# Kernel tuning notes

Measured on AMD Instinct MI355X. Metric: run time of the kernel, lower is better.

Reference implementation:

```python
import jax, jax.numpy as jnp
import numpy as np

N = 8192
IN_C, HID_C, OUT_C = 128, 256, 128


def setup_inputs() -> dict:
    key = jax.random.key(0)
    ks = jax.random.split(key, 6)
    return {
        "x": jax.random.normal(ks[0], (N, IN_C), dtype=jnp.float32),
        "adaptive_params": jax.random.normal(ks[1], (N, N), dtype=jnp.float32),
        "W1": jax.random.normal(ks[2], (IN_C, HID_C), dtype=jnp.float32) * (1.0 / np.sqrt(IN_C)),
        "b1": jax.random.normal(ks[3], (HID_C,), dtype=jnp.float32) * 0.01,
        "W2": jax.random.normal(ks[4], (HID_C, OUT_C), dtype=jnp.float32) * (1.0 / np.sqrt(HID_C)),
        "b2": jax.random.normal(ks[5], (OUT_C,), dtype=jnp.float32) * 0.01,
    }


def _normalized_adj(adaptive_params):
    # initial_adj = I; A = sigmoid(sym(I + P)) where sym(M) = (M + M^T)/2
    n = adaptive_params.shape[0]
    eye = jnp.eye(n, dtype=adaptive_params.dtype)
    sym = eye + 0.5 * (adaptive_params + adaptive_params.T)
    A = jax.nn.sigmoid(sym)
    # sigmoid > 0 everywhere -> edge_index covers all N^2 pairs (dense graph).
    # PyG gcn_norm (add_self_loops=True, fill_value=1.0): A_hat = A + I,
    # then symmetric degree normalization D^-1/2 A_hat D^-1/2.
    A_hat = A + eye
    dinv = jax.lax.rsqrt(jnp.sum(A_hat, axis=1))  # [N]
    return A_hat * dinv[:, None] * dinv[None, :]


def reference(x, adaptive_params, W1, b1, W2, b2):
    A_norm = _normalized_adj(adaptive_params)          # [N, N]
    h = jax.nn.relu(A_norm @ (x @ W1) + b1)            # [N, HID_C]
    out = A_norm @ (h @ W2) + b2                       # [N, OUT_C]
    return out
```

## Files before the change

### kernel.cpp

```cpp
#include <hip/hip_runtime.h>
#include <hip/hip_bf16.h>
#include <cstdint>

typedef unsigned short u16;
typedef unsigned short u16x4 __attribute__((ext_vector_type(4)));
typedef unsigned short u16x8 __attribute__((ext_vector_type(8)));
typedef _Float16 f16x8 __attribute__((ext_vector_type(8)));
typedef float f32x4 __attribute__((ext_vector_type(4)));

constexpr int NN   = 8192;
constexpr int INC  = 128;
constexpr int HIDC = 256;
constexpr int OUTC = 128;
constexpr int KSPLIT = 8;

__device__ __forceinline__ u16 f2h(float f) {
    _Float16 h = (_Float16)f;
    return __builtin_bit_cast(u16, h);
}
__device__ __forceinline__ float h2f(u16 u) {
    return (float)__builtin_bit_cast(_Float16, u);
}
__device__ __forceinline__ float fast_sigmoid(float z) {
    float e;
    asm("v_exp_f32 %0, %1" : "=v"(e) : "v"(z * -1.44269504088896f));
    float s;
    asm("v_rcp_f32 %0, %1" : "=v"(s) : "v"(1.0f + e));
    return s;
}

typedef __attribute__((address_space(1))) const void* gptr_t;
typedef __attribute__((address_space(3))) void* sptr_t;
#define GLD16(g, s) __builtin_amdgcn_global_load_lds((gptr_t)(g), (sptr_t)(s), 16, 0, 0)

__global__ __launch_bounds__(512, 4) void k_adj(const float* __restrict__ P,
                                                u16* __restrict__ AH,
                                                float* __restrict__ psum,
                                                const float* __restrict__ W2,
                                                u16* __restrict__ W2T) {
    const int t = threadIdx.x;
    if (blockIdx.x == 0) {
        for (int e = t; e < OUTC * HIDC; e += 512) {
            int c = e >> 8, k = e & 255;
            W2T[c * HIDC + k] = f2h(W2[k * OUTC + c]);
        }
        return;
    }
    int bid = blockIdx.x - 1;
    int bi, bj;
    if (bid >= 2016)      { bi = bj = bid - 2016; }
    else if (bid >= 1984) { bi = 31; bj = 32 + (bid - 1984); }
    else {
        int u = bid >> 6, v = bid & 63;
        if (v < 63 - u) { bi = u;      bj = u + 1 + v; }
        else            { bi = 62 - u; bj = v; }
    }
    constexpr int LW = 136;
    __shared__ u16 hB[128 * LW];
    __shared__ float cs[8][128];
    const int i0 = bi * 128, j0 = bj * 128;
    const bool diag = (bi == bj);

    #pragma unroll
    for (int p = 0; p < 4; ++p) {
        int idx = p * 512 + t;
        int r = idx >> 4, m = idx & 15;
        const float* pb = P + (size_t)(j0 + r) * NN + i0 + m * 8;
        f32x4 b0 = __builtin_nontemporal_load((const f32x4*)pb);
        f32x4 b1 = __builtin_nontemporal_load((const f32x4*)(pb + 4));
        u16x8 hb;
        hb[0] = f2h(b0[0]); hb[1] = f2h(b0[1]); hb[2] = f2h(b0[2]); hb[3] = f2h(b0[3]);
        hb[4] = f2h(b1[0]); hb[5] = f2h(b1[1]); hb[6] = f2h(b1[2]); hb[7] = f2h(b1[3]);
        int pos = m ^ ((r >> 3) & 7);
        *(u16x8*)&hB[r * LW + pos * 8] = hb;
    }

    const int rb = t >> 4, cb = t & 15;
    const int R = rb * 4, C = cb * 8;
    f32x4 a0[4], a1[4];
    #pragma unroll
    for (int i = 0; i < 4; ++i) {
        const float* pa = P + (size_t)(i0 + R + i) * NN + j0 + C;
        a0[i] = __builtin_nontemporal_load((const f32x4*)pa);
        a1[i] = __builtin_nontemporal_load((const f32x4*)(pa + 4));
    }
    __syncthreads();

    float rsum[4] = {0.f, 0.f, 0.f, 0.f};
    float csum[8] = {0.f, 0.f, 0.f, 0.f, 0.f, 0.f, 0.f, 0.f};
    u16x4 mir[8];
    {
        u16x4 bv[8];
        #pragma unroll
        for (int j = 0; j < 8; ++j) {
            int r = C + j;
            int pos = (rb >> 1) ^ (cb & 7);
            bv[j] = *(const u16x4*)&hB[r * LW + pos * 8 + (rb & 1) * 4];
        }
        #pragma unroll
        for (int i = 0; i < 4; ++i) {
            u16x8 o;
            #pragma unroll
            for (int j = 0; j < 8; ++j) {
                float av = (j < 4) ? a0[i][j] : a1[i][j - 4];
                float z = 0.5f * (av + h2f(bv[j][i]));
                bool dg = (i0 + R + i) == (j0 + C + j);
                if (dg) z += 1.0f;
                float s = fast_sigmoid(z);
                if (dg) s += 1.0f;
                u16 h = f2h(s);
                o[j] = h;
                mir[j][i] = h;
                rsum[i] += s;
                csum[j] += s;
            }
            *(u16x8*)(AH + (size_t)(i0 + R + i) * NN + j0 + C) = o;
        }
        if (!diag) {
            #pragma unroll
            for (int j = 0; j < 8; ++j) {
                int r = C + j;
                int pos = (rb >> 1) ^ (cb & 7);
                *(u16x4*)&hB[r * LW + pos * 8 + (rb & 1) * 4] = mir[j];
            }
        }
    }

    #pragma unroll
    for (int m = 1; m <= 8; m <<= 1) {
        #pragma unroll
        for (int i = 0; i < 4; ++i) rsum[i] += __shfl_xor(rsum[i], m);
    }
    if (cb == 0) {
        f32x4 rv = {rsum[0], rsum[1], rsum[2], rsum[3]};
        *(f32x4*)&psum[(size_t)bj * NN + i0 + R] = rv;
    }

    if (!diag) {
        #pragma unroll
        for (int j = 0; j < 8; ++j) {
            csum[j] += __shfl_xor(csum[j], 16);
            csum[j] += __shfl_xor(csum[j], 32);
        }
        const int w = t >> 6;
        if ((t & 48) == 0) {
            #pragma unroll
            for (int j = 0; j < 8; ++j) cs[w][C + j] = csum[j];
        }
    }
    __syncthreads();

    if (!diag) {
        const int r2 = t >> 4, m = t & 15;
        #pragma unroll
        for (int p = 0; p < 4; ++p) {
            int rr = r2 + p * 32;
            int pos = m ^ ((rr >> 3) & 7);
            *(u16x8*)(AH + (size_t)(j0 + rr) * NN + i0 + m * 8) =
                *(const u16x8*)&hB[rr * LW + pos * 8];
        }
        if (t < 128) {
            float s = 0.f;
            #pragma unroll
            for (int k = 0; k < 8; ++k) s += cs[k][t];
            psum[(size_t)bi * NN + j0 + t] = s;
        }
    }
}

__global__ __launch_bounds__(256) void k_xw1(const float* __restrict__ x,
                                             const float* __restrict__ W1,
                                             const float* __restrict__ psum,
                                             float* __restrict__ rowsum,
                                             u16* __restrict__ XW1T) {
    const int t = threadIdx.x;
    __shared__ float xs[32 * 129];
    __shared__ float rs_s[32];
    const int i0 = blockIdx.x * 32;
    if (t < 32) {
        float rs = 0.f;
        #pragma unroll 8
        for (int v = 0; v < 64; ++v) rs += psum[(size_t)v * NN + i0 + t];
        rs_s[t] = rs;
        rowsum[i0 + t] = rs;
    }
    #pragma unroll
    for (int p = 0; p < 4; ++p) {
        int idx = p * 256 + t;
        int r = idx >> 5, c4 = idx & 31;
        f32x4 v = __builtin_nontemporal_load(
            (const f32x4*)(x + (size_t)(i0 + r) * INC + c4 * 4));
        int o = r * 129 + c4 * 4;
        xs[o] = v[0]; xs[o + 1] = v[1]; xs[o + 2] = v[2]; xs[o + 3] = v[3];
    }
    __syncthreads();
    const int i = t & 31, g = t >> 5;
    const float di = 1.0f / sqrtf(rs_s[i]);
    #pragma unroll
    for (int p = 0; p < 2; ++p) {
        const int cbase = g * 32 + p * 16;
        float acc[16];
        #pragma unroll
        for (int cc = 0; cc < 16; ++cc) acc[cc] = 0.f;
        for (int k = 0; k < 128; ++k) {
            float xv = xs[i * 129 + k];
            const float4* wr4 = reinterpret_cast<const float4*>(W1 + k * HIDC + cbase);
            float4 w0 = wr4[0], w1 = wr4[1], w2 = wr4[2], w3 = wr4[3];
            acc[0]  = fmaf(xv, w0.x, acc[0]);  acc[1]  = fmaf(xv, w0.y, acc[1]);
            acc[2]  = fmaf(xv, w0.z, acc[2]);  acc[3]  = fmaf(xv, w0.w, acc[3]);
            acc[4]  = fmaf(xv, w1.x, acc[4]);  acc[5]  = fmaf(xv, w1.y, acc[5]);
            acc[6]  = fmaf(xv, w1.z, acc[6]);  acc[7]  = fmaf(xv, w1.w, acc[7]);
            acc[8]  = fmaf(xv, w2.x, acc[8]);  acc[9]  = fmaf(xv, w2.y, acc[9]);
            acc[10] = fmaf(xv, w2.z, acc[10]); acc[11] = fmaf(xv, w2.w, acc[11]);
            acc[12] = fmaf(xv, w3.x, acc[12]); acc[13] = fmaf(xv, w3.y, acc[13]);
            acc[14] = fmaf(xv, w3.z, acc[14]); acc[15] = fmaf(xv, w3.w, acc[15]);
        }
        #pragma unroll
        for (int cc = 0; cc < 16; ++cc)
            XW1T[(size_t)(cbase + cc) * NN + i0 + i] = f2h(di * acc[cc]);
    }
}

#define PH_MID() do { __builtin_amdgcn_s_barrier();                             \
    asm volatile("s_waitcnt lgkmcnt(0)" ::: "memory");                          \
    __builtin_amdgcn_sched_barrier(0);                                          \
    __builtin_amdgcn_s_setprio(1); } while (0)

#define PH_NW() do { __builtin_amdgcn_s_setprio(0);                             \
    __builtin_amdgcn_s_barrier(); } while (0)

#define PH_W() do { __builtin_amdgcn_s_setprio(0);                              \
    if constexpr (BN == 256) { asm volatile("s_waitcnt vmcnt(6)" ::: "memory"); } \
    else                     { asm volatile("s_waitcnt vmcnt(4)" ::: "memory"); } \
    __builtin_amdgcn_s_barrier(); } while (0)

#define PH_W0() do { __builtin_amdgcn_s_setprio(0);                             \
    asm volatile("s_waitcnt vmcnt(0)" ::: "memory");                            \
    __builtin_amdgcn_s_barrier(); } while (0)

template <int BN>
__global__ __launch_bounds__(512, 2) void k_gemm8(const u16* __restrict__ A,
                                                  const u16* __restrict__ BT,
                                                  u16* __restrict__ partial) {
    constexpr int NI = BN / 128;
    constexpr int NQB = BN / 64;
    constexpr int BUFB = BN * 128;
    constexpr int KCH = NN / KSPLIT;
    constexpr int NT = KCH / 64;
    constexpr int ITER = NT / 2;
    __shared__ __align__(16) char lds[65536 + 2 * BUFB];

    const int t = threadIdx.x;
    const int l = t & 63, w = t >> 6;
    const int wr = w >> 2, wc = w & 3;
    const int g2 = (blockIdx.x & 7) * 32 + (blockIdx.x >> 3);
    const int m0 = (g2 & 31) * 256;
    const int kc = g2 >> 5;
    const int kbase = kc * KCH;

    const int D16 = t * 16;
    const int Ds = D16 ^ (((D16 >> 7) & 7) << 4);
    const int rS = Ds >> 7, cS = (Ds & 127) >> 1;

    f32x4 acc[8][NI * 2];
    #pragma unroll
    for (int i = 0; i < 8; ++i)
        #pragma unroll
        for (int j = 0; j < NI * 2; ++j) acc[i][j] = {0.f, 0.f, 0.f, 0.f};

    f16x8 a[4][2];
    f16x8 bf[2][NI][2];

    auto stageA = [&](int b, int q, int tile) {
        GLD16(A + (size_t)(m0 + q * 64 + rS) * NN + kbase + tile * 64 + cS,
              &lds[b * 32768 + q * 8192 + D16]);
    };
    auto stageB = [&](int b, int q, int tile) {
        GLD16(BT + (size_t)(q * 64 + rS) * NN + kbase + tile * 64 + cS,
              &lds[65536 + b * BUFB + q * 8192 + D16]);
    };
    auto readA = [&](int b, int mh) {
        #pragma unroll
        for (int mi = 0; mi < 4; ++mi)
            #pragma unroll
            for (int s = 0; s < 2; ++s) {
                int r = wr * 128 + mh * 64 + mi * 16 + (l & 15);
                a[mi][s] = *(const f16x8*)&lds[b * 32768 + r * 128 +
                    ((s * 64 + ((l >> 4) * 16)) ^ ((r & 7) << 4))];
            }
    };
    auto readB = [&](int b, int nh) {
        #pragma unroll
        for (int ni = 0; ni < NI; ++ni)
            #pragma unroll
            for (int s = 0; s < 2; ++s) {
                int r = wc * (BN / 4) + nh * (NI * 16) + ni * 16 + (l & 15);
                bf[nh][ni][s] = *(const f16x8*)&lds[65536 + b * BUFB + r * 128 +
                    ((s * 64 + ((l >> 4) * 16)) ^ ((r & 7) << 4))];
            }
    };
    auto mfmaq = [&](int mh, int nh) {
        #pragma unroll
        for (int s = 0; s < 2; ++s)
            #pragma unroll
            for (int mi = 0; mi < 4; ++mi)
                #pragma unroll
                for (int ni = 0; ni < NI; ++ni)
                    acc[mh * 4 + mi][nh * NI + ni] =
                        __builtin_amdgcn_mfma_f32_16x16x32_f16(a[mi][s], bf[nh][ni][s],
                            acc[mh * 4 + mi][nh * NI + ni], 0, 0, 0);
    };

    #pragma unroll
    for (int q = 0; q < NQB; ++q) stageB(0, q, 0);
    #pragma unroll
    for (int q = 0; q < 4; ++q) stageA(0, q, 0);
    #pragma unroll
    for (int q = 0; q < NQB; ++q) stageB(1, q, 1);
    stageA(1, 0, 1); stageA(1, 1, 1);
    if constexpr (BN == 256) { asm volatile("s_waitcnt vmcnt(6)" ::: "memory"); }
    else                     { asm volatile("s_waitcnt vmcnt(4)" ::: "memory"); }
    __builtin_amdgcn_s_barrier();

    for (int it = 0; it < ITER - 1; ++it) {
        const int TP = 2 * it + 1, TE = 2 * it + 2, TO = 2 * it + 3;
        readA(0, 0); readB(0, 0); stageA(1, 2, TP); stageA(1, 3, TP);
        PH_MID(); mfmaq(0, 0); PH_NW();
        readB(0, 1);
        PH_MID(); mfmaq(0, 1); PH_NW();
        readA(0, 1); stageB(0, 0, TE); stageB(0, 1, TE);
        PH_MID(); mfmaq(1, 0); PH_NW();
        if constexpr (BN == 256) { stageB(0, 2, TE); stageB(0, 3, TE); }
        stageA(0, 0, TE); stageA(0, 1, TE);
        PH_MID(); mfmaq(1, 1); PH_W();
        readA(1, 0); readB(1, 0); stageA(0, 2, TE); stageA(0, 3, TE);
        PH_MID(); mfmaq(0, 0); PH_NW();
        readB(1, 1);
        PH_MID(); mfmaq(0, 1); PH_NW();
        readA(1, 1); stageB(1, 0, TO); stageB(1, 1, TO);
        PH_MID(); mfmaq(1, 0); PH_NW();
        if constexpr (BN == 256) { stageB(1, 2, TO); stageB(1, 3, TO); }
        stageA(1, 0, TO); stageA(1, 1, TO);
        PH_MID(); mfmaq(1, 1); PH_W();
    }
    readA(0, 0); readB(0, 0); stageA(1, 2, NT - 1); stageA(1, 3, NT - 1);
    PH_MID(); mfmaq(0, 0); PH_NW();
    readB(0, 1);
    PH_MID(); mfmaq(0, 1); PH_NW();
    readA(0, 1);
    PH_MID(); mfmaq(1, 0); PH_NW();
    PH_MID(); mfmaq(1, 1); PH_W0();
    readA(1, 0); readB(1, 0);
    PH_MID(); mfmaq(0, 0); PH_NW();
    readB(1, 1);
    PH_MID(); mfmaq(0, 1); PH_NW();
    readA(1, 1);
    PH_MID(); mfmaq(1, 0); PH_NW();
    PH_MID(); mfmaq(1, 1);
    __builtin_amdgcn_s_setprio(0);

    u16* pout = partial + (size_t)kc * NN * BN;
    #pragma unroll
    for (int mh = 0; mh < 2; ++mh)
        #pragma unroll
        for (int mi = 0; mi < 4; ++mi)
            #pragma unroll
            for (int j = 0; j < 4; ++j) {
                int grow = m0 + wr * 128 + mh * 64 + mi * 16 + (l >> 4) * 4 + j;
                #pragma unroll
                for (int nh = 0; nh < 2; ++nh)
                    #pragma unroll
                    for (int ni = 0; ni < NI; ++ni) {
                        int gcol = wc * (BN / 4) + nh * (NI * 16) + ni * 16 + (l & 15);
                        pout[(size_t)grow * BN + gcol] = f2h(acc[mh * 4 + mi][nh * NI + ni][j]);
                    }
            }
}

__global__ __launch_bounds__(512) void k_epi1hw2m(const u16* __restrict__ partial,
                                                  const float* __restrict__ rowsum,
                                                  const float* __restrict__ b1,
                                                  const u16* __restrict__ W2T,
                                                  u16* __restrict__ HW2T) {
    __shared__ __align__(16) char lds[81920];
    const int t = threadIdx.x;
    const int l = t & 63, w = t >> 6;
    const int i0 = blockIdx.x * 32;

    #pragma unroll
    for (int p = 0; p < 8; ++p) {
        int D = (p * 512 + t) * 16;
        int row = D >> 9;
        int col = (D & 511) ^ ((row & 7) << 4);
        GLD16(W2T + (size_t)row * HIDC + (col >> 1), &lds[D]);
    }
    #pragma unroll
    for (int p = 0; p < 2; ++p) {
        int qi = p * 512 + t;
        int i = qi >> 5, cq = qi & 31;
        float s[8] = {0.f, 0.f, 0.f, 0.f, 0.f, 0.f, 0.f, 0.f};
        #pragma unroll
        for (int kc = 0; kc < KSPLIT; ++kc) {
            u16x8 pv = __builtin_nontemporal_load(
                (const u16x8*)(partial + ((size_t)kc * NN + i0 + i) * HIDC + cq * 8));
            #pragma unroll
            for (int k = 0; k < 8; ++k) s[k] += h2f(pv[k]);
        }
        const float di = 1.0f / sqrtf(rowsum[i0 + i]);
        u16x8 o;
        #pragma unroll
        for (int k = 0; k < 8; ++k)
            o[k] = f2h(di * fmaxf(fmaf(di, s[k], b1[cq * 8 + k]), 0.f));
        *(u16x8*)&lds[65536 + i * 512 + ((cq * 16) ^ ((i & 7) << 4))] = o;
    }
    asm volatile("s_waitcnt vmcnt(0)" ::: "memory");
    __syncthreads();

    const int wm = w >> 1, wn = w & 1;
    f32x4 acc[2];
    acc[0] = {0.f, 0.f, 0.f, 0.f}; acc[1] = {0.f, 0.f, 0.f, 0.f};
    for (int kt = 0; kt < 8; ++kt) {
        f16x8 av[2], bv;
        const int cb2 = kt * 64 + (l >> 4) * 16;
        #pragma unroll
        for (int mi = 0; mi < 2; ++mi) {
            int r = wm * 32 + mi * 16 + (l & 15);
            av[mi] = *(const f16x8*)&lds[r * 512 + (cb2 ^ ((r & 7) << 4))];
        }
        {
            int ri = wn * 16 + (l & 15);
            bv = *(const f16x8*)&lds[65536 + ri * 512 + (cb2 ^ ((ri & 7) << 4))];
        }
        #pragma unroll
        for (int mi = 0; mi < 2; ++mi)
            acc[mi] = __builtin_amdgcn_mfma_f32_16x16x32_f16(av[mi], bv, acc[mi], 0, 0, 0);
    }
    #pragma unroll
    for (int mi = 0; mi < 2; ++mi)
        #pragma unroll
        for (int j = 0; j < 4; ++j) {
            int c = wm * 32 + mi * 16 + (l >> 4) * 4 + j;
            int ic = wn * 16 + (l & 15);
            HW2T[(size_t)c * NN + i0 + ic] = f2h(acc[mi][j]);
        }
}

__global__ __launch_bounds__(256) void k_epi2(const u16* __restrict__ partial,
                                              const float* __restrict__ rowsum,
                                              const float* __restrict__ b2,
                                              float* __restrict__ out) {
    const int idx = blockIdx.x * 256 + threadIdx.x;
    const int i = idx >> 4, cq = idx & 15;
    float s[8] = {0.f, 0.f, 0.f, 0.f, 0.f, 0.f, 0.f, 0.f};
    #pragma unroll
    for (int kc = 0; kc < KSPLIT; ++kc) {
        u16x8 pv = __builtin_nontemporal_load(
            (const u16x8*)(partial + ((size_t)kc * NN + i) * OUTC + cq * 8));
        #pragma unroll
        for (int k = 0; k < 8; ++k) s[k] += h2f(pv[k]);
    }
    const float di = 1.0f / sqrtf(rowsum[i]);
    float o[8];
    #pragma unroll
    for (int k = 0; k < 8; ++k) o[k] = fmaf(di, s[k], b2[cq * 8 + k]);
    float* op = out + (size_t)i * OUTC + cq * 8;
    *reinterpret_cast<float4*>(op) = make_float4(o[0], o[1], o[2], o[3]);
    *reinterpret_cast<float4*>(op + 4) = make_float4(o[4], o[5], o[6], o[7]);
}

extern "C" void kernel_launch(void* const* d_in, const int* in_sizes, int n_in,
                              void* d_out, int out_size, void* d_ws, size_t ws_size,
                              hipStream_t stream) {
    const float* x  = (const float*)d_in[0];
    const float* P  = (const float*)d_in[1];
    const float* W1 = (const float*)d_in[2];
    const float* b1 = (const float*)d_in[3];
    const float* W2 = (const float*)d_in[4];
    const float* b2 = (const float*)d_in[5];
    float* out = (float*)d_out;
    char* ws = (char*)d_ws;

    u16*   AH      = (u16*)(ws);
    u16*   XW1T    = (u16*)(ws + 134217728ull);
    u16*   W2T     = (u16*)(ws + 138412032ull);
    u16*   HW2T    = (u16*)(ws + 138477568ull);
    float* rowsum  = (float*)(ws + 140574720ull);
    u16*   partial = (u16*)(ws + 140607488ull);
    float* psum    = (float*)(ws + 174161920ull);

    k_adj<<<2081, 512, 0, stream>>>(P, AH, psum, W2, W2T);
    k_xw1<<<256, 256, 0, stream>>>(x, W1, psum, rowsum, XW1T);
    k_gemm8<HIDC><<<256, 512, 0, stream>>>(AH, XW1T, partial);
    k_epi1hw2m<<<256, 512, 0, stream>>>(partial, rowsum, b1, W2T, HW2T);
    k_gemm8<OUTC><<<256, 512, 0, stream>>>(AH, HW2T, partial);
    k_epi2<<<512, 256, 0, stream>>>(partial, rowsum, b2, out);
}
```

Baseline: 196.3 us.

## Store split-K partials in MFMA fragment order with vectorized writes

The GEMM epilogue now writes each accumulator fragment as one contiguous 8-byte u16x4 per lane in a fragment-ordered layout, replacing scattered 2-byte stores across rows. Both reduction kernels (epi1 and epi2) are rewritten to decode this layout, loading 16 contiguous halfs per split, and epi2 now handles four rows by four columns per thread with half as many blocks. This is meant to cut uncoalesced store traffic from the large GEMMs, at the cost of more complex index math and scalar 2-byte LDS writes in epi1.

```diff
diff --git a/kernel.cpp b/kernel.cpp
--- a/kernel.cpp
+++ b/kernel.cpp
@@ -359,22 +359,22 @@
     PH_MID(); mfmaq(1, 1);
     __builtin_amdgcn_s_setprio(0);
 
-    u16* pout = partial + (size_t)kc * NN * BN;
+    u16* pout = partial + (size_t)kc * NN * BN + (size_t)(g2 & 31) * (256 * BN);
     #pragma unroll
     for (int mh = 0; mh < 2; ++mh)
         #pragma unroll
         for (int mi = 0; mi < 4; ++mi)
             #pragma unroll
-            for (int j = 0; j < 4; ++j) {
-                int grow = m0 + wr * 128 + mh * 64 + mi * 16 + (l >> 4) * 4 + j;
+            for (int nh = 0; nh < 2; ++nh)
                 #pragma unroll
-                for (int nh = 0; nh < 2; ++nh)
+                for (int ni = 0; ni < NI; ++ni) {
+                    int f = (((w * 2 + mh) * 4 + mi) * 2 + nh) * NI + ni;
+                    u16x4 v;
                     #pragma unroll
-                    for (int ni = 0; ni < NI; ++ni) {
-                        int gcol = wc * (BN / 4) + nh * (NI * 16) + ni * 16 + (l & 15);
-                        pout[(size_t)grow * BN + gcol] = f2h(acc[mh * 4 + mi][nh * NI + ni][j]);
-                    }
-            }
+                    for (int j = 0; j < 4; ++j)
+                        v[j] = f2h(acc[mh * 4 + mi][nh * NI + ni][j]);
+                    *(u16x4*)(pout + ((size_t)f * 64 + l) * 4) = v;
+                }
 }
 
 __global__ __launch_bounds__(512) void k_epi1hw2m(const u16* __restrict__ partial,
@@ -394,24 +394,41 @@
         int col = (D & 511) ^ ((row & 7) << 4);
         GLD16(W2T + (size_t)row * HIDC + (col >> 1), &lds[D]);
     }
-    #pragma unroll
-    for (int p = 0; p < 2; ++p) {
-        int qi = p * 512 + t;
-        int i = qi >> 5, cq = qi & 31;
-        float s[8] = {0.f, 0.f, 0.f, 0.f, 0.f, 0.f, 0.f, 0.f};
+
+    {
+        const int rq = w;
+        const int c = l * 4;
+        const int cl = c & 15, ni = (c >> 4) & 1, nh = (c >> 5) & 1, wcq = c >> 6;
+        const int lr0 = i0 & 255;
+        const int wrq = lr0 >> 7, mhq = (lr0 >> 6) & 1;
+        const int mi = ((lr0 >> 4) & 3) + (rq >> 2);
+        const int lgrp = rq & 3;
+        const int mb = i0 >> 8;
+        const int f = ((((wrq * 4 + wcq) * 2 + mhq) * 4 + mi) * 2 + nh) * 2 + ni;
+        const size_t boff = (size_t)mb * 65536 + ((size_t)f * 64 + lgrp * 16 + cl) * 4;
+        float s[16];
+        #pragma unroll
+        for (int e = 0; e < 16; ++e) s[e] = 0.f;
         #pragma unroll
         for (int kc = 0; kc < KSPLIT; ++kc) {
-            u16x8 pv = __builtin_nontemporal_load(
-                (const u16x8*)(partial + ((size_t)kc * NN + i0 + i) * HIDC + cq * 8));
-            #pragma unroll
-            for (int k = 0; k < 8; ++k) s[k] += h2f(pv[k]);
-        }
-        const float di = 1.0f / sqrtf(rowsum[i0 + i]);
-        u16x8 o;
-        #pragma unroll
-        for (int k = 0; k < 8; ++k)
-            o[k] = f2h(di * fmaxf(fmaf(di, s[k], b1[cq * 8 + k]), 0.f));
-        *(u16x8*)&lds[65536 + i * 512 + ((cq * 16) ^ ((i & 7) << 4))] = o;
+            const u16* src = partial + (size_t)kc * NN * HIDC + boff;
+            u16x8 p0 = __builtin_nontemporal_load((const u16x8*)src);
+            u16x8 p1 = __builtin_nontemporal_load((const u16x8*)(src + 8));
+            #pragma unroll
+            for (int e = 0; e < 8; ++e) { s[e] += h2f(p0[e]); s[8 + e] += h2f(p1[e]); }
+        }
+        float di[4];
+        #pragma unroll
+        for (int j = 0; j < 4; ++j) di[j] = 1.0f / sqrtf(rowsum[i0 + rq * 4 + j]);
+        f32x4 b1v = *(const f32x4*)(b1 + c);
+        #pragma unroll
+        for (int k = 0; k < 4; ++k)
+            #pragma unroll
+            for (int j = 0; j < 4; ++j) {
+                float hv = di[j] * fmaxf(fmaf(di[j], s[k * 4 + j], b1v[k]), 0.f);
+                int il = rq * 4 + j;
+                *(u16*)&lds[65536 + il * 512 + ((2 * (c + k)) ^ ((il & 7) << 4))] = f2h(hv);
+            }
     }
     asm volatile("s_waitcnt vmcnt(0)" ::: "memory");
     __syncthreads();
@@ -450,22 +467,37 @@
                                               const float* __restrict__ b2,
                                               float* __restrict__ out) {
     const int idx = blockIdx.x * 256 + threadIdx.x;
-    const int i = idx >> 4, cq = idx & 15;
-    float s[8] = {0.f, 0.f, 0.f, 0.f, 0.f, 0.f, 0.f, 0.f};
+    const int rq = idx >> 5;
+    const int c4g = idx & 31;
+    const int c = c4g * 4;
+    const int cl = c & 15, nh = (c >> 4) & 1, wc = c >> 5;
+    const int mb = rq >> 6;
+    const int lr4 = rq & 63;
+    const int wr = lr4 >> 5, mh = (lr4 >> 4) & 1, mi = (lr4 >> 2) & 3, lgrp = lr4 & 3;
+    const int f = (((wr * 4 + wc) * 2 + mh) * 4 + mi) * 2 + nh;
+    const size_t boff = (size_t)mb * 32768 + ((size_t)f * 64 + lgrp * 16 + cl) * 4;
+    float s[16];
+    #pragma unroll
+    for (int e = 0; e < 16; ++e) s[e] = 0.f;
     #pragma unroll
     for (int kc = 0; kc < KSPLIT; ++kc) {
-        u16x8 pv = __builtin_nontemporal_load(
-            (const u16x8*)(partial + ((size_t)kc * NN + i) * OUTC + cq * 8));
-        #pragma unroll
-        for (int k = 0; k < 8; ++k) s[k] += h2f(pv[k]);
-    }
-    const float di = 1.0f / sqrtf(rowsum[i]);
-    float o[8];
-    #pragma unroll
-    for (int k = 0; k < 8; ++k) o[k] = fmaf(di, s[k], b2[cq * 8 + k]);
-    float* op = out + (size_t)i * OUTC + cq * 8;
-    *reinterpret_cast<float4*>(op) = make_float4(o[0], o[1], o[2], o[3]);
-    *reinterpret_cast<float4*>(op + 4) = make_float4(o[4], o[5], o[6], o[7]);
+        const u16* src = partial + (size_t)kc * NN * OUTC + boff;
+        u16x8 p0 = __builtin_nontemporal_load((const u16x8*)src);
+        u16x8 p1 = __builtin_nontemporal_load((const u16x8*)(src + 8));
+        #pragma unroll
+        for (int e = 0; e < 8; ++e) { s[e] += h2f(p0[e]); s[8 + e] += h2f(p1[e]); }
+    }
+    const int i_base = rq * 4;
+    f32x4 b2v = *(const f32x4*)(b2 + c);
+    #pragma unroll
+    for (int j = 0; j < 4; ++j) {
+        const float di = 1.0f / sqrtf(rowsum[i_base + j]);
+        float4 o = make_float4(fmaf(di, s[0 * 4 + j], b2v[0]),
+                               fmaf(di, s[1 * 4 + j], b2v[1]),
+                               fmaf(di, s[2 * 4 + j], b2v[2]),
+                               fmaf(di, s[3 * 4 + j], b2v[3]));
+        *reinterpret_cast<float4*>(out + (size_t)(i_base + j) * OUTC + c) = o;
+    }
 }
 
 extern "C" void kernel_launch(void* const* d_in, const int* in_sizes, int n_in,
@@ -493,5 +525,5 @@
     k_gemm8<HIDC><<<256, 512, 0, stream>>>(AH, XW1T, partial);
     k_epi1hw2m<<<256, 512, 0, stream>>>(partial, rowsum, b1, W2T, HW2T);
     k_gemm8<OUTC><<<256, 512, 0, stream>>>(AH, HW2T, partial);
-    k_epi2<<<512, 256, 0, stream>>>(partial, rowsum, b2, out);
-}
+    k_epi2<<<256, 256, 0, stream>>>(partial, rowsum, b2, out);
+}
```

New measurement: 195.2 us (median of 2 runs). Within noise of the previous version (-0.5%).
